# Performance work log

Measured on AMD Instinct MI355X. Metric: run time of the kernel, lower is better.

## Reference

```python
import jax, jax.numpy as jnp
import numpy as np

N_CLASSES = 256
MAX_SQRT_BETA = 1.0
MIN_SQRT_BETA = 1e-10
EPSILON = 1e-06


def setup_inputs() -> dict:
    key = jax.random.key(0)
    k1, k2, k3 = jax.random.split(key, 3)
    B, S = 8, 2048
    data = jax.random.randint(k1, (B, S), 0, N_CLASSES)          # class indices
    t = jax.random.uniform(k2, (B, S), dtype=jnp.float32)        # time in [0,1)
    noise = jax.random.normal(k3, (B, S, N_CLASSES), dtype=jnp.float32)  # std normal for MVN rsample
    return {"data": data, "t": t, "noise": noise}


def reference(data, t, noise):
    K = N_CLASSES
    # scheduler == 'square': sqrt_beta = t * max_sqrt_beta
    sqrt_beta = jnp.clip(t, None, 1.0 - EPSILON) * MAX_SQRT_BETA
    lo_beta = sqrt_beta < MIN_SQRT_BETA
    sqrt_beta = jnp.clip(sqrt_beta, MIN_SQRT_BETA, None)
    beta = (sqrt_beta * sqrt_beta)[..., None]                    # [B,S,1]

    # count_dist: mean = beta * (K * one_hot(x) - 1)
    e_x = jax.nn.one_hot(data, K, dtype=jnp.float32)             # [B,S,K]
    mean = beta * (K * e_x - 1.0)

    # cov = beta * C0, C0 = K*I - 11^T + 0.001*I  (equicorrelated)
    C0 = (K + 0.001) * jnp.eye(K, dtype=jnp.float32) - jnp.ones((K, K), jnp.float32)
    L0 = jnp.linalg.cholesky(C0)                                 # [K,K] lower
    # MVN rsample: mean + L @ eps, with L = sqrt(beta) * L0
    logits = mean + jnp.sqrt(beta) * jnp.einsum('bsk,jk->bsj', noise, L0)

    probs = jax.nn.softmax(logits, axis=-1)
    probs = jnp.where(lo_beta[..., None], jnp.full_like(probs, 1.0 / K), probs)
    return probs
```

## Files before the change

### kernel.cpp

```cpp
#include <hip/hip_runtime.h>
#include <math.h>


#define NCLS 256

__global__ __launch_bounds__(256) void dbf_kernel(
    const int* __restrict__ data,
    const float* __restrict__ t,
    const float4* __restrict__ noise4,
    float4* __restrict__ out4,
    int n_rows)
{
    __shared__ float4 s_b4[64];
    __shared__ float4 s_a4[64];
    {
        const int k = threadIdx.x;
        const double d = 256.001;
        const double tk = d / ((double)k - d);
        const double ak = sqrt(d + tk);
        ((float*)s_a4)[k] = (float)ak;
        ((float*)s_b4)[k] = (float)(tk / ak);
    }
    __syncthreads();

    const int lane = threadIdx.x & 63;
    const int wave = threadIdx.x >> 6;
    const int row  = blockIdx.x * 4 + wave;
    if (row >= n_rows) return;

    const float4 nz = noise4[(size_t)row * 64 + lane];
    const float4 bv = s_b4[lane];
    const float4 av = s_a4[lane];

    const float w0 = nz.x * bv.x;
    const float w1 = nz.y * bv.y;
    const float w2 = nz.z * bv.z;
    const float w3 = nz.w * bv.w;
    const float local = w0 + w1 + w2 + w3;

    float v = local;
    #pragma unroll
    for (int off = 1; off < 64; off <<= 1) {
        float n = __shfl_up(v, off, 64);
        if (lane >= off) v += n;
    }
    const float base = v - local;

    const float tt = t[row];
    float sb = fminf(tt, 1.0f - 1e-6f);
    const bool lo = sb < 1e-10f;
    sb = fmaxf(sb, 1e-10f);
    const float beta = sb * sb;
    const int  x = data[row];

    const int j0 = lane * 4;
    const float dot0 = base + nz.x * av.x;
    const float dot1 = base + w0 + nz.y * av.y;
    const float dot2 = base + w0 + w1 + nz.z * av.z;
    const float dot3 = base + w0 + w1 + w2 + nz.w * av.w;

    float l0 = beta * (256.0f * (float)(j0 + 0 == x) - 1.0f) + sb * dot0;
    float l1 = beta * (256.0f * (float)(j0 + 1 == x) - 1.0f) + sb * dot1;
    float l2 = beta * (256.0f * (float)(j0 + 2 == x) - 1.0f) + sb * dot2;
    float l3 = beta * (256.0f * (float)(j0 + 3 == x) - 1.0f) + sb * dot3;

    float m = fmaxf(fmaxf(l0, l1), fmaxf(l2, l3));
    #pragma unroll
    for (int off = 32; off > 0; off >>= 1)
        m = fmaxf(m, __shfl_xor(m, off, 64));

    const float e0 = expf(l0 - m);
    const float e1 = expf(l1 - m);
    const float e2 = expf(l2 - m);
    const float e3 = expf(l3 - m);
    float s = e0 + e1 + e2 + e3;
    #pragma unroll
    for (int off = 32; off > 0; off >>= 1)
        s += __shfl_xor(s, off, 64);
    const float inv = 1.0f / s;

    float4 o;
    if (lo) {
        const float u = 1.0f / 256.0f;
        o.x = u; o.y = u; o.z = u; o.w = u;
    } else {
        o.x = e0 * inv; o.y = e1 * inv; o.z = e2 * inv; o.w = e3 * inv;
    }
    out4[(size_t)row * 64 + lane] = o;
}

extern "C" void kernel_launch(void* const* d_in, const int* in_sizes, int n_in,
                              void* d_out, int out_size, void* d_ws, size_t ws_size,
                              hipStream_t stream) {
    const int*    data   = (const int*)d_in[0];
    const float*  t      = (const float*)d_in[1];
    const float4* noise4 = (const float4*)d_in[2];
    float4*       out4   = (float4*)d_out;

    const int n_rows = in_sizes[1];
    const int blocks = (n_rows + 3) / 4;
    dbf_kernel<<<blocks, 256, 0, stream>>>(data, t, noise4, out4, n_rows);
}
```

Measured before the change: 77.09 us.

## Process two rows per wave with DPP scans and per-lane Cholesky coefficients

Each wave now handles two rows, and their noise, t and data loads are issued together up front to raise memory-level parallelism. The prefix scan and the max/sum reductions use DPP row operations plus readlane instead of ds_bpermute-based shuffles. The Cholesky coefficients are computed per lane in double precision in registers instead of through shared memory with a block barrier, and exp is computed via exp2f. The block count halves, and the per-lane double-precision divides and sqrts now run in every wave rather than once per block.

```diff
diff --git a/kernel.cpp b/kernel.cpp
--- a/kernel.cpp
+++ b/kernel.cpp
@@ -2,7 +2,38 @@
 #include <math.h>
 
 
-#define NCLS 256
+#define ROWS_PER_WAVE 2
+
+template<int CTRL, int RM>
+__device__ __forceinline__ float dpp_f(float oldv, float x) {
+    return __int_as_float(__builtin_amdgcn_update_dpp(
+        __float_as_int(oldv), __float_as_int(x), CTRL, RM, 0xF, false));
+}
+
+__device__ __forceinline__ float wave_iscan_add(float x) {
+    x += dpp_f<0x111, 0xF>(0.0f, x);
+    x += dpp_f<0x112, 0xF>(0.0f, x);
+    x += dpp_f<0x114, 0xF>(0.0f, x);
+    x += dpp_f<0x118, 0xF>(0.0f, x);
+    x += dpp_f<0x142, 0xA>(0.0f, x);
+    x += dpp_f<0x143, 0xC>(0.0f, x);
+    return x;
+}
+
+__device__ __forceinline__ float wave_bcast_sum(float x) {
+    x = wave_iscan_add(x);
+    return __int_as_float(__builtin_amdgcn_readlane(__float_as_int(x), 63));
+}
+
+__device__ __forceinline__ float wave_bcast_max(float x) {
+    x = fmaxf(x, dpp_f<0x111, 0xF>(x, x));
+    x = fmaxf(x, dpp_f<0x112, 0xF>(x, x));
+    x = fmaxf(x, dpp_f<0x114, 0xF>(x, x));
+    x = fmaxf(x, dpp_f<0x118, 0xF>(x, x));
+    x = fmaxf(x, dpp_f<0x142, 0xA>(x, x));
+    x = fmaxf(x, dpp_f<0x143, 0xC>(x, x));
+    return __int_as_float(__builtin_amdgcn_readlane(__float_as_int(x), 63));
+}
 
 __global__ __launch_bounds__(256) void dbf_kernel(
     const int* __restrict__ data,
@@ -11,82 +42,76 @@
     float4* __restrict__ out4,
     int n_rows)
 {
-    __shared__ float4 s_b4[64];
-    __shared__ float4 s_a4[64];
-    {
-        const int k = threadIdx.x;
-        const double d = 256.001;
-        const double tk = d / ((double)k - d);
-        const double ak = sqrt(d + tk);
-        ((float*)s_a4)[k] = (float)ak;
-        ((float*)s_b4)[k] = (float)(tk / ak);
-    }
-    __syncthreads();
-
     const int lane = threadIdx.x & 63;
     const int wave = threadIdx.x >> 6;
-    const int row  = blockIdx.x * 4 + wave;
-    if (row >= n_rows) return;
+    const int row0 = (blockIdx.x * 4 + wave) * ROWS_PER_WAVE;
+    if (row0 >= n_rows) return;
 
-    const float4 nz = noise4[(size_t)row * 64 + lane];
-    const float4 bv = s_b4[lane];
-    const float4 av = s_a4[lane];
+    float av[4], bv[4];
+    #pragma unroll
+    for (int i = 0; i < 4; ++i) {
+        const double d = 256.001;
+        const double tk = d / ((double)(lane * 4 + i) - d);
+        const double a = sqrt(d + tk);
+        av[i] = (float)a;
+        bv[i] = (float)(tk / a);
+    }
 
-    const float w0 = nz.x * bv.x;
-    const float w1 = nz.y * bv.y;
-    const float w2 = nz.z * bv.z;
-    const float w3 = nz.w * bv.w;
-    const float local = w0 + w1 + w2 + w3;
+    float4 nz[ROWS_PER_WAVE];
+    float  tt[ROWS_PER_WAVE];
+    int    xx[ROWS_PER_WAVE];
+    bool   ok[ROWS_PER_WAVE];
+    #pragma unroll
+    for (int r = 0; r < ROWS_PER_WAVE; ++r) {
+        const int row = row0 + r;
+        ok[r] = (row < n_rows);
+        const int rr = ok[r] ? row : 0;
+        nz[r] = noise4[(size_t)rr * 64 + lane];
+        tt[r] = t[rr];
+        xx[r] = data[rr];
+    }
 
-    float v = local;
     #pragma unroll
-    for (int off = 1; off < 64; off <<= 1) {
-        float n = __shfl_up(v, off, 64);
-        if (lane >= off) v += n;
+    for (int r = 0; r < ROWS_PER_WAVE; ++r) {
+        if (!ok[r]) continue;
+        const float w0 = nz[r].x * bv[0];
+        const float w1 = nz[r].y * bv[1];
+        const float w2 = nz[r].z * bv[2];
+        const float w3 = nz[r].w * bv[3];
+        const float local = w0 + w1 + w2 + w3;
+        const float base  = wave_iscan_add(local) - local;
+
+        float sb = fminf(tt[r], 1.0f - 1e-6f);
+        const bool lo = sb < 1e-10f;
+        sb = fmaxf(sb, 1e-10f);
+        const float beta = sb * sb;
+        const int x = xx[r];
+        const int j0 = lane * 4;
+
+        float l0 = beta * (256.0f * (float)(j0 + 0 == x) - 1.0f) + sb * (base + nz[r].x * av[0]);
+        float l1 = beta * (256.0f * (float)(j0 + 1 == x) - 1.0f) + sb * (base + w0 + nz[r].y * av[1]);
+        float l2 = beta * (256.0f * (float)(j0 + 2 == x) - 1.0f) + sb * (base + w0 + w1 + nz[r].z * av[2]);
+        float l3 = beta * (256.0f * (float)(j0 + 3 == x) - 1.0f) + sb * (base + w0 + w1 + w2 + nz[r].w * av[3]);
+
+        const float m = wave_bcast_max(fmaxf(fmaxf(l0, l1), fmaxf(l2, l3)));
+
+        const float LOG2E = 1.4426950408889634f;
+        const float e0 = exp2f((l0 - m) * LOG2E);
+        const float e1 = exp2f((l1 - m) * LOG2E);
+        const float e2 = exp2f((l2 - m) * LOG2E);
+        const float e3 = exp2f((l3 - m) * LOG2E);
+        const float s = wave_bcast_sum(e0 + e1 + e2 + e3);
+        const float inv = 1.0f / s;
+
+        float4 o;
+        if (lo) {
+            const float u = 1.0f / 256.0f;
+            o.x = u; o.y = u; o.z = u; o.w = u;
+        } else {
+            o.x = e0 * inv; o.y = e1 * inv; o.z = e2 * inv; o.w = e3 * inv;
+        }
+        out4[(size_t)(row0 + r) * 64 + lane] = o;
     }
-    const float base = v - local;
-
-    const float tt = t[row];
-    float sb = fminf(tt, 1.0f - 1e-6f);
-    const bool lo = sb < 1e-10f;
-    sb = fmaxf(sb, 1e-10f);
-    const float beta = sb * sb;
-    const int  x = data[row];
-
-    const int j0 = lane * 4;
-    const float dot0 = base + nz.x * av.x;
-    const float dot1 = base + w0 + nz.y * av.y;
-    const float dot2 = base + w0 + w1 + nz.z * av.z;
-    const float dot3 = base + w0 + w1 + w2 + nz.w * av.w;
-
-    float l0 = beta * (256.0f * (float)(j0 + 0 == x) - 1.0f) + sb * dot0;
-    float l1 = beta * (256.0f * (float)(j0 + 1 == x) - 1.0f) + sb * dot1;
-    float l2 = beta * (256.0f * (float)(j0 + 2 == x) - 1.0f) + sb * dot2;
-    float l3 = beta * (256.0f * (float)(j0 + 3 == x) - 1.0f) + sb * dot3;
-
-    float m = fmaxf(fmaxf(l0, l1), fmaxf(l2, l3));
-    #pragma unroll
-    for (int off = 32; off > 0; off >>= 1)
-        m = fmaxf(m, __shfl_xor(m, off, 64));
-
-    const float e0 = expf(l0 - m);
-    const float e1 = expf(l1 - m);
-    const float e2 = expf(l2 - m);
-    const float e3 = expf(l3 - m);
-    float s = e0 + e1 + e2 + e3;
-    #pragma unroll
-    for (int off = 32; off > 0; off >>= 1)
-        s += __shfl_xor(s, off, 64);
-    const float inv = 1.0f / s;
-
-    float4 o;
-    if (lo) {
-        const float u = 1.0f / 256.0f;
-        o.x = u; o.y = u; o.z = u; o.w = u;
-    } else {
-        o.x = e0 * inv; o.y = e1 * inv; o.z = e2 * inv; o.w = e3 * inv;
-    }
-    out4[(size_t)row * 64 + lane] = o;
 }
 
 extern "C" void kernel_launch(void* const* d_in, const int* in_sizes, int n_in,
@@ -98,6 +123,7 @@
     float4*       out4   = (float4*)d_out;
 
     const int n_rows = in_sizes[1];
-    const int blocks = (n_rows + 3) / 4;
+    const int rows_per_block = 4 * ROWS_PER_WAVE;
+    const int blocks = (n_rows + rows_per_block - 1) / rows_per_block;
     dbf_kernel<<<blocks, 256, 0, stream>>>(data, t, noise4, out4, n_rows);
 }
```

Measured after the change: 76.65 us. Within noise of the previous version (-0.6%).
